# Performance work log

Hardware: AMD Instinct MI355X
Metric: run time of the kernel (lower is better)

The kernel has to match this reference:

```python
import jax, jax.numpy as jnp
import numpy as np
import math

S, B, H, NH = 2048, 1, 4096, 32
D = H // NH  # 128 head dim


def rotate_half(x):
    x1, x2 = x[..., : x.shape[-1] // 2], x[..., x.shape[-1] // 2 :]
    return jnp.concatenate((-x2, x1), axis=-1)


def setup_inputs() -> dict:
    key = jax.random.key(0)
    k1, k2, k3, k4, k5 = jax.random.split(key, 5)
    hidden_states = jax.random.normal(k1, (S, B, H), dtype=jnp.float32)
    position_ids = jnp.broadcast_to(jnp.arange(S, dtype=jnp.int32)[None, :], (B, S))
    # causal mask: True = masked (upper triangle above diagonal)
    attention_mask = jnp.triu(jnp.ones((S, S), dtype=bool), k=1)[None, None]
    W_qkv = jax.random.normal(k2, (H, 3 * H), dtype=jnp.float32) * 0.02
    b_qkv = jax.random.normal(k3, (3 * H,), dtype=jnp.float32) * 0.02
    W_dense = jax.random.normal(k4, (H, H), dtype=jnp.float32) * 0.02
    b_dense = jax.random.normal(k5, (H,), dtype=jnp.float32) * 0.02
    return {
        "hidden_states": hidden_states,
        "position_ids": position_ids,
        "attention_mask": attention_mask,
        "W_qkv": W_qkv,
        "b_qkv": b_qkv,
        "W_dense": W_dense,
        "b_dense": b_dense,
        "layer_id": 27,
    }


def reference(hidden_states, position_ids, attention_mask, W_qkv, b_qkv, W_dense, b_dense, layer_id):
    s, b, h = hidden_states.shape
    nh, d = NH, D
    # QKV projection: [s, b, 3h] -> [s, b, nh, 3d] -> split
    mixed = hidden_states @ W_qkv + b_qkv
    mixed = mixed.reshape(s, b, nh, 3 * d)
    q, k, v = jnp.split(mixed, 3, axis=-1)  # each [s, b, nh, d]
    # rotary embedding indexed by position_ids (transposed to [s, b])
    pos = position_ids.T  # [s, b]
    inv_freq = 1.0 / (10000.0 ** (jnp.arange(0, d, 2, dtype=jnp.float32) / d))
    freqs = pos[..., None].astype(jnp.float32) * inv_freq  # [s, b, d/2]
    emb = jnp.concatenate((freqs, freqs), axis=-1)  # [s, b, d]
    cos = jnp.cos(emb)[:, :, None, :]  # [s, b, 1, d]
    sin = jnp.sin(emb)[:, :, None, :]
    q = q * cos + rotate_half(q) * sin
    k = k * cos + rotate_half(k) * sin
    # attention with per-layer scaling coeff (cancels in softmax except mask fill)
    coeff = jnp.float32(layer_id + 1)
    q_scaled = q / (math.sqrt(d) * coeff)
    scores = jnp.einsum("sbnd,tbnd->bnst", q_scaled, k)  # [b, nh, s, s]
    scores = jnp.where(attention_mask, jnp.float32(-10000.0), scores) * coeff
    probs = jax.nn.softmax(scores, axis=-1)
    ctx = jnp.einsum("bnst,tbnd->sbnd", probs, v).reshape(s, b, h)
    out = ctx @ W_dense + b_dense
    return out
```

## Files before the change

kernel.cpp:

```cpp
#include <hip/hip_runtime.h>

#define S_LEN 2048
#define HID   4096
#define NHEAD 32
#define DHEAD 128
#define H3    12288

typedef __attribute__((ext_vector_type(8))) __bf16 bf16x8;
typedef __attribute__((ext_vector_type(4))) __bf16 bf16x4;
typedef __attribute__((ext_vector_type(4))) float  f32x4;

__device__ __forceinline__ void gl_lds16(const void* g, void* l) {
  __builtin_amdgcn_global_load_lds(
      (const __attribute__((address_space(1))) void*)g,
      (__attribute__((address_space(3))) void*)l, 16, 0, 0);
}

__global__ void cvt_f32_bf16(const float* __restrict__ in, __bf16* __restrict__ out, int n4) {
  int i = blockIdx.x * blockDim.x + threadIdx.x;
  if (i >= n4) return;
  float4 v = ((const float4*)in)[i];
  bf16x4 o;
  o.x = (__bf16)v.x; o.y = (__bf16)v.y; o.z = (__bf16)v.z; o.w = (__bf16)v.w;
  ((bf16x4*)out)[i] = o;
}

__global__ void transpose_cvt(const float* __restrict__ in, __bf16* __restrict__ out, int R, int C) {
  __shared__ float t[64][65];
  const int tid = threadIdx.x;
  const int r0 = blockIdx.y * 64, c0 = blockIdx.x * 64;
#pragma unroll
  for (int p = 0; p < 4; ++p) {
    int r = p * 16 + (tid >> 4);
    int c4 = (tid & 15) * 4;
    float4 v = *(const float4*)(in + (size_t)(r0 + r) * C + c0 + c4);
    t[r][c4] = v.x; t[r][c4 + 1] = v.y; t[r][c4 + 2] = v.z; t[r][c4 + 3] = v.w;
  }
  __syncthreads();
#pragma unroll
  for (int p = 0; p < 4; ++p) {
    int c = p * 16 + (tid >> 4);
    int rg = (tid & 15) * 4;
    bf16x4 o;
    o.x = (__bf16)t[rg][c]; o.y = (__bf16)t[rg + 1][c];
    o.z = (__bf16)t[rg + 2][c]; o.w = (__bf16)t[rg + 3][c];
    *(bf16x4*)(out + (size_t)(c0 + c) * R + r0 + rg) = o;
  }
}

__global__ void rope_kernel(__bf16* __restrict__ q, __bf16* __restrict__ k,
                            const int* __restrict__ pos) {
  int idx = blockIdx.x * 256 + threadIdx.x;
  int j = idx & 63;
  int hs = idx >> 6;
  int s = hs & (S_LEN - 1);
  float p = (float)pos[s];
  float invf = __expf(-(float)j * (9.210340371976184f / 64.f));
  float a = p * invf;
  float c, sn;
  __sincosf(a, &sn, &c);
  size_t base = (size_t)hs * 128;
  float x1 = (float)q[base + j], x2 = (float)q[base + j + 64];
  q[base + j]      = (__bf16)(x1 * c - x2 * sn);
  q[base + j + 64] = (__bf16)(x2 * c + x1 * sn);
  x1 = (float)k[base + j]; x2 = (float)k[base + j + 64];
  k[base + j]      = (__bf16)(x1 * c - x2 * sn);
  k[base + j + 64] = (__bf16)(x2 * c + x1 * sn);
}

template <int EPI>
__global__ __launch_bounds__(256, 2)
void gemm_bf16(const __bf16* __restrict__ A, const __bf16* __restrict__ BT,
               const float* __restrict__ bias, int K,
               __bf16* __restrict__ outq, __bf16* __restrict__ outk,
               __bf16* __restrict__ outvt, float* __restrict__ outf) {
  const int tid = threadIdx.x;
  const int lane = tid & 63;
  const int wave = tid >> 6;
  const int bm = blockIdx.x * 128;
  const int bn = blockIdx.y * 128;

  __shared__ __bf16 As[128 * 64];
  __shared__ __bf16 Bs[128 * 64];
  char* Ab = (char*)As;
  char* Bb = (char*)Bs;

  f32x4 acc[4][4] = {};

  const int wm = (wave >> 1) * 64;
  const int wn = (wave & 1) * 64;

  const int sr = tid >> 3;
  const int sc = (tid & 7) * 16;
  const int scs = sc ^ ((sr & 7) << 4);

  const char* Arow = (const char*)(A + (size_t)(bm + sr) * K) + scs;
  const char* Brow = (const char*)(BT + (size_t)(bn + sr) * K) + scs;

  for (int k0 = 0; k0 < K; k0 += 64) {
    const char* a_src = Arow + (size_t)k0 * 2;
    const char* b_src = Brow + (size_t)k0 * 2;
    char* a_dst = Ab + wave * 1024;
    char* b_dst = Bb + wave * 1024;
#pragma unroll
    for (int i = 0; i < 4; ++i) {
      gl_lds16(a_src + (size_t)i * 32 * K * 2, a_dst + i * 4096);
      gl_lds16(b_src + (size_t)i * 32 * K * 2, b_dst + i * 4096);
    }
    __syncthreads();
#pragma unroll
    for (int kk = 0; kk < 2; ++kk) {
      bf16x8 af[4], bfr[4];
#pragma unroll
      for (int m = 0; m < 4; ++m) {
        int row = wm + m * 16 + (lane & 15);
        int cb = (kk * 64 + ((lane >> 4) << 4)) ^ ((row & 7) << 4);
        af[m] = *(const bf16x8*)(Ab + row * 128 + cb);
      }
#pragma unroll
      for (int n = 0; n < 4; ++n) {
        int row = wn + n * 16 + (lane & 15);
        int cb = (kk * 64 + ((lane >> 4) << 4)) ^ ((row & 7) << 4);
        bfr[n] = *(const bf16x8*)(Bb + row * 128 + cb);
      }
#pragma unroll
      for (int m = 0; m < 4; ++m)
#pragma unroll
        for (int n = 0; n < 4; ++n)
          acc[m][n] = __builtin_amdgcn_mfma_f32_16x16x32_bf16(af[m], bfr[n], acc[m][n], 0, 0, 0);
    }
    __syncthreads();
  }

  const int rbase = (lane >> 4) << 2;
  const int cl = lane & 15;
  if (EPI == 0) {
    const int route = (bn >> 7) % 3;
    const int head = bn / 384;
#pragma unroll
    for (int n = 0; n < 4; ++n) {
      const int d = wn + n * 16 + cl;
      const float bv = bias[bn + d];
#pragma unroll
      for (int m = 0; m < 4; ++m) {
        const int srow = bm + wm + m * 16 + rbase;
        if (route == 2) {
          bf16x4 o;
          o.x = (__bf16)(acc[m][n][0] + bv);
          o.y = (__bf16)(acc[m][n][1] + bv);
          o.z = (__bf16)(acc[m][n][2] + bv);
          o.w = (__bf16)(acc[m][n][3] + bv);
          *(bf16x4*)(outvt + ((size_t)head * 128 + d) * S_LEN + srow) = o;
        } else {
          __bf16* dst = (route == 0 ? outq : outk) + (size_t)head * S_LEN * 128;
#pragma unroll
          for (int r = 0; r < 4; ++r)
            dst[(size_t)(srow + r) * 128 + d] = (__bf16)(acc[m][n][r] + bv);
        }
      }
    }
  } else {
#pragma unroll
    for (int n = 0; n < 4; ++n) {
      const int col = bn + wn + n * 16 + cl;
      const float bv = bias[col];
#pragma unroll
      for (int m = 0; m < 4; ++m) {
        const int srow = bm + wm + m * 16 + rbase;
#pragma unroll
        for (int r = 0; r < 4; ++r)
          outf[(size_t)(srow + r) * HID + col] = acc[m][n][r] + bv;
      }
    }
  }
}

__global__ __launch_bounds__(256, 2)
void attn_kernel(const __bf16* __restrict__ q, const __bf16* __restrict__ k,
                 const __bf16* __restrict__ vt, __bf16* __restrict__ ctx) {
  const int qb = blockIdx.x, h = blockIdx.y;
  const int tid = threadIdx.x, lane = tid & 63, wave = tid >> 6;
  __shared__ __bf16 Ks[64 * 128];
  __shared__ __bf16 Vs[128 * 64];
  __shared__ __bf16 Ps[4][32 * 64];
  char* Kb = (char*)Ks;
  char* Vb = (char*)Vs;
  char* Pb = (char*)(Ps[wave]);

  const __bf16* qh = q + (size_t)h * S_LEN * 128;
  const __bf16* kh = k + (size_t)h * S_LEN * 128;
  const __bf16* vh = vt + (size_t)h * 128 * S_LEN;

  const int qrow0 = qb * 128 + wave * 32;
  const int cl = lane & 15, rbase = (lane >> 4) << 2;

  bf16x8 qf[2][4];
#pragma unroll
  for (int m = 0; m < 2; ++m)
#pragma unroll
    for (int kk = 0; kk < 4; ++kk)
      qf[m][kk] = *(const bf16x8*)(qh + (size_t)(qrow0 + m * 16 + cl) * 128 + kk * 32 + ((lane >> 4) << 3));

  f32x4 oacc[2][8] = {};
  float mrow[2][4], lrow[2][4];
#pragma unroll
  for (int m = 0; m < 2; ++m)
#pragma unroll
    for (int r = 0; r < 4; ++r) { mrow[m][r] = -1e30f; lrow[m][r] = 0.f; }

  const int krow = tid >> 4, kcol = (tid & 15) * 16;
  const int kcs = kcol ^ ((krow & 7) << 4);
  const int vrow = tid >> 3, vcol = (tid & 7) * 16;
  const int vcs = vcol ^ ((vrow & 7) << 4);

  const int nT = 2 * qb + 2;
  for (int t = 0; t < nT; ++t) {
    {
      const char* src = (const char*)(kh + (size_t)(t * 64 + krow) * 128) + kcs;
      char* dst = Kb + wave * 1024;
#pragma unroll
      for (int i = 0; i < 4; ++i)
        gl_lds16(src + (size_t)i * 16 * 256, dst + i * 4096);
    }
    {
      const char* src = (const char*)(vh + (size_t)vrow * S_LEN + t * 64) + vcs;
      char* dst = Vb + wave * 1024;
#pragma unroll
      for (int i = 0; i < 4; ++i)
        gl_lds16(src + (size_t)i * 32 * (S_LEN * 2), dst + i * 4096);
    }
    __syncthreads();
    if (t * 64 <= qrow0 + 31) {
      f32x4 sacc[2][4] = {};
#pragma unroll
      for (int kk = 0; kk < 4; ++kk) {
        bf16x8 bk[4];
#pragma unroll
        for (int n = 0; n < 4; ++n) {
          int row = n * 16 + cl;
          int cb = (kk * 64 + ((lane >> 4) << 4)) ^ ((row & 7) << 4);
          bk[n] = *(const bf16x8*)(Kb + row * 256 + cb);
        }
#pragma unroll
        for (int m = 0; m < 2; ++m)
#pragma unroll
          for (int n = 0; n < 4; ++n)
            sacc[m][n] = __builtin_amdgcn_mfma_f32_16x16x32_bf16(qf[m][kk], bk[n], sacc[m][n], 0, 0, 0);
      }
#pragma unroll
      for (int m = 0; m < 2; ++m) {
        float pmax[4];
#pragma unroll
        for (int r = 0; r < 4; ++r) pmax[r] = -1e30f;
#pragma unroll
        for (int n = 0; n < 4; ++n) {
          const int col = t * 64 + n * 16 + cl;
#pragma unroll
          for (int r = 0; r < 4; ++r) {
            const int row = qrow0 + m * 16 + rbase + r;
            float sv = sacc[m][n][r] * 0.08838834764831845f;
            sv = (col > row) ? -1e30f : sv;
            sacc[m][n][r] = sv;
            pmax[r] = fmaxf(pmax[r], sv);
          }
        }
#pragma unroll
        for (int xm = 1; xm < 16; xm <<= 1)
#pragma unroll
          for (int r = 0; r < 4; ++r)
            pmax[r] = fmaxf(pmax[r], __shfl_xor(pmax[r], xm, 64));
#pragma unroll
        for (int r = 0; r < 4; ++r) {
          const float mnew = fmaxf(mrow[m][r], pmax[r]);
          const float alpha = __expf(mrow[m][r] - mnew);
          mrow[m][r] = mnew;
          float psum = 0.f;
#pragma unroll
          for (int n = 0; n < 4; ++n) {
            float p = __expf(sacc[m][n][r] - mnew);
            sacc[m][n][r] = p;
            psum += p;
          }
#pragma unroll
          for (int xm = 1; xm < 16; xm <<= 1)
            psum += __shfl_xor(psum, xm, 64);
          lrow[m][r] = lrow[m][r] * alpha + psum;
#pragma unroll
          for (int nd = 0; nd < 8; ++nd)
            oacc[m][nd][r] *= alpha;
        }
#pragma unroll
        for (int n = 0; n < 4; ++n) {
          const int colb = (n * 16 + cl) * 2;
#pragma unroll
          for (int r = 0; r < 4; ++r) {
            const int row = m * 16 + rbase + r;
            *(__bf16*)(Pb + row * 128 + (colb ^ ((row & 7) << 4))) = (__bf16)sacc[m][n][r];
          }
        }
      }
#pragma unroll
      for (int kk = 0; kk < 2; ++kk) {
        bf16x8 pa[2], bv[8];
#pragma unroll
        for (int m = 0; m < 2; ++m) {
          int row = m * 16 + cl;
          int cb = (kk * 64 + ((lane >> 4) << 4)) ^ ((row & 7) << 4);
          pa[m] = *(const bf16x8*)(Pb + row * 128 + cb);
        }
#pragma unroll
        for (int nd = 0; nd < 8; ++nd) {
          int row = nd * 16 + cl;
          int cb = (kk * 64 + ((lane >> 4) << 4)) ^ ((row & 7) << 4);
          bv[nd] = *(const bf16x8*)(Vb + row * 128 + cb);
        }
#pragma unroll
        for (int m = 0; m < 2; ++m)
#pragma unroll
          for (int nd = 0; nd < 8; ++nd)
            oacc[m][nd] = __builtin_amdgcn_mfma_f32_16x16x32_bf16(pa[m], bv[nd], oacc[m][nd], 0, 0, 0);
      }
    }
    __syncthreads();
  }
#pragma unroll
  for (int m = 0; m < 2; ++m)
#pragma unroll
    for (int nd = 0; nd < 8; ++nd) {
      const int d = nd * 16 + cl;
#pragma unroll
      for (int r = 0; r < 4; ++r) {
        const int srow = qrow0 + m * 16 + rbase + r;
        ctx[(size_t)srow * HID + h * 128 + d] = (__bf16)(oacc[m][nd][r] / lrow[m][r]);
      }
    }
}

extern "C" void kernel_launch(void* const* d_in, const int* in_sizes, int n_in,
                              void* d_out, int out_size, void* d_ws, size_t ws_size,
                              hipStream_t stream) {
  const float* hs = (const float*)d_in[0];
  const int* pos = (const int*)d_in[1];
  const float* wqkv = (const float*)d_in[3];
  const float* bqkv = (const float*)d_in[4];
  const float* wd = (const float*)d_in[5];
  const float* bd = (const float*)d_in[6];
  float* out = (float*)d_out;

  char* ws = (char*)d_ws;
  const size_t MB = 1024ull * 1024ull;
  if (ws_size < 160 * MB) return;
  __bf16* wT  = (__bf16*)(ws);
  __bf16* xb  = (__bf16*)(ws + 96 * MB);
  __bf16* qb_ = (__bf16*)(ws + 112 * MB);
  __bf16* kb_ = (__bf16*)(ws + 128 * MB);
  __bf16* vtb = (__bf16*)(ws + 144 * MB);

  cvt_f32_bf16<<<8192, 256, 0, stream>>>(hs, xb, 2097152);
  transpose_cvt<<<dim3(192, 64), 256, 0, stream>>>(wqkv, wT, 4096, 12288);
  gemm_bf16<0><<<dim3(16, 96), 256, 0, stream>>>(xb, wT, bqkv, 4096, qb_, kb_, vtb, nullptr);
  rope_kernel<<<16384, 256, 0, stream>>>(qb_, kb_, pos);
  transpose_cvt<<<dim3(64, 64), 256, 0, stream>>>(wd, wT, 4096, 4096);
  attn_kernel<<<dim3(16, 32), 256, 0, stream>>>(qb_, kb_, vtb, xb);
  gemm_bf16<1><<<dim3(16, 32), 256, 0, stream>>>(xb, wT, bd, 4096, nullptr, nullptr, nullptr, out);
}
```

Baseline: 509.5 us.

## Pair causal query tiles per attention block to balance work across blocks

Each attention block now handles two 64-row query tiles, p and 31-p, one after the other, instead of one 128-row tile. Every block therefore does about the same number of key tiles, removing the causal triangle's imbalance where late blocks set the critical path. Each wave now owns 16 query rows rather than 32, and the causal mask is applied only on the diagonal tile. In exchange, each loaded K/V tile is reused by fewer query rows, so MFMA work per sync and per LDS load is lower.

```diff
diff --git a/kernel.cpp b/kernel.cpp
--- a/kernel.cpp
+++ b/kernel.cpp
@@ -178,11 +178,11 @@
 __global__ __launch_bounds__(256, 2)
 void attn_kernel(const __bf16* __restrict__ q, const __bf16* __restrict__ k,
                  const __bf16* __restrict__ vt, __bf16* __restrict__ ctx) {
-  const int qb = blockIdx.x, h = blockIdx.y;
+  const int p = blockIdx.x, h = blockIdx.y;
   const int tid = threadIdx.x, lane = tid & 63, wave = tid >> 6;
   __shared__ __bf16 Ks[64 * 128];
   __shared__ __bf16 Vs[128 * 64];
-  __shared__ __bf16 Ps[4][32 * 64];
+  __shared__ __bf16 Ps[4][16 * 64];
   char* Kb = (char*)Ks;
   char* Vb = (char*)Vs;
   char* Pb = (char*)(Ps[wave]);
@@ -191,47 +191,45 @@
   const __bf16* kh = k + (size_t)h * S_LEN * 128;
   const __bf16* vh = vt + (size_t)h * 128 * S_LEN;
 
-  const int qrow0 = qb * 128 + wave * 32;
   const int cl = lane & 15, rbase = (lane >> 4) << 2;
-
-  bf16x8 qf[2][4];
-#pragma unroll
-  for (int m = 0; m < 2; ++m)
-#pragma unroll
-    for (int kk = 0; kk < 4; ++kk)
-      qf[m][kk] = *(const bf16x8*)(qh + (size_t)(qrow0 + m * 16 + cl) * 128 + kk * 32 + ((lane >> 4) << 3));
-
-  f32x4 oacc[2][8] = {};
-  float mrow[2][4], lrow[2][4];
-#pragma unroll
-  for (int m = 0; m < 2; ++m)
-#pragma unroll
-    for (int r = 0; r < 4; ++r) { mrow[m][r] = -1e30f; lrow[m][r] = 0.f; }
 
   const int krow = tid >> 4, kcol = (tid & 15) * 16;
   const int kcs = kcol ^ ((krow & 7) << 4);
   const int vrow = tid >> 3, vcol = (tid & 7) * 16;
   const int vcs = vcol ^ ((vrow & 7) << 4);
 
-  const int nT = 2 * qb + 2;
-  for (int t = 0; t < nT; ++t) {
-    {
-      const char* src = (const char*)(kh + (size_t)(t * 64 + krow) * 128) + kcs;
-      char* dst = Kb + wave * 1024;
-#pragma unroll
-      for (int i = 0; i < 4; ++i)
-        gl_lds16(src + (size_t)i * 16 * 256, dst + i * 4096);
-    }
-    {
-      const char* src = (const char*)(vh + (size_t)vrow * S_LEN + t * 64) + vcs;
-      char* dst = Vb + wave * 1024;
-#pragma unroll
-      for (int i = 0; i < 4; ++i)
-        gl_lds16(src + (size_t)i * 32 * (S_LEN * 2), dst + i * 4096);
-    }
-    __syncthreads();
-    if (t * 64 <= qrow0 + 31) {
-      f32x4 sacc[2][4] = {};
+  for (int half = 0; half < 2; ++half) {
+    const int qt = half ? (31 - p) : p;
+    const int qrow0 = qt * 64 + wave * 16;
+
+    bf16x8 qf[4];
+#pragma unroll
+    for (int kk = 0; kk < 4; ++kk)
+      qf[kk] = *(const bf16x8*)(qh + (size_t)(qrow0 + cl) * 128 + kk * 32 + ((lane >> 4) << 3));
+
+    f32x4 oacc[8] = {};
+    float mrow[4], lrow[4];
+#pragma unroll
+    for (int r = 0; r < 4; ++r) { mrow[r] = -1e30f; lrow[r] = 0.f; }
+
+    for (int j = 0; j <= qt; ++j) {
+      {
+        const char* src = (const char*)(kh + (size_t)(j * 64 + krow) * 128) + kcs;
+        char* dst = Kb + wave * 1024;
+#pragma unroll
+        for (int i = 0; i < 4; ++i)
+          gl_lds16(src + (size_t)i * 16 * 256, dst + i * 4096);
+      }
+      {
+        const char* src = (const char*)(vh + (size_t)vrow * S_LEN + j * 64) + vcs;
+        char* dst = Vb + wave * 1024;
+#pragma unroll
+        for (int i = 0; i < 4; ++i)
+          gl_lds16(src + (size_t)i * 32 * (S_LEN * 2), dst + i * 4096);
+      }
+      __syncthreads();
+
+      f32x4 sacc[4] = {};
 #pragma unroll
       for (int kk = 0; kk < 4; ++kk) {
         bf16x8 bk[4];
@@ -242,71 +240,79 @@
           bk[n] = *(const bf16x8*)(Kb + row * 256 + cb);
         }
 #pragma unroll
-        for (int m = 0; m < 2; ++m)
-#pragma unroll
-          for (int n = 0; n < 4; ++n)
-            sacc[m][n] = __builtin_amdgcn_mfma_f32_16x16x32_bf16(qf[m][kk], bk[n], sacc[m][n], 0, 0, 0);
-      }
-#pragma unroll
-      for (int m = 0; m < 2; ++m) {
-        float pmax[4];
-#pragma unroll
-        for (int r = 0; r < 4; ++r) pmax[r] = -1e30f;
+        for (int n = 0; n < 4; ++n)
+          sacc[n] = __builtin_amdgcn_mfma_f32_16x16x32_bf16(qf[kk], bk[n], sacc[n], 0, 0, 0);
+      }
+
+      float pmax[4];
+#pragma unroll
+      for (int r = 0; r < 4; ++r) pmax[r] = -1e30f;
+      if (j == qt) {
 #pragma unroll
         for (int n = 0; n < 4; ++n) {
-          const int col = t * 64 + n * 16 + cl;
+          const int col = n * 16 + cl;
 #pragma unroll
           for (int r = 0; r < 4; ++r) {
-            const int row = qrow0 + m * 16 + rbase + r;
-            float sv = sacc[m][n][r] * 0.08838834764831845f;
+            const int row = wave * 16 + rbase + r;
+            float sv = sacc[n][r] * 0.08838834764831845f;
             sv = (col > row) ? -1e30f : sv;
-            sacc[m][n][r] = sv;
+            sacc[n][r] = sv;
             pmax[r] = fmaxf(pmax[r], sv);
           }
         }
+      } else {
+#pragma unroll
+        for (int n = 0; n < 4; ++n)
+#pragma unroll
+          for (int r = 0; r < 4; ++r) {
+            float sv = sacc[n][r] * 0.08838834764831845f;
+            sacc[n][r] = sv;
+            pmax[r] = fmaxf(pmax[r], sv);
+          }
+      }
+#pragma unroll
+      for (int xm = 1; xm < 16; xm <<= 1)
+#pragma unroll
+        for (int r = 0; r < 4; ++r)
+          pmax[r] = fmaxf(pmax[r], __shfl_xor(pmax[r], xm, 64));
+#pragma unroll
+      for (int r = 0; r < 4; ++r) {
+        const float mnew = fmaxf(mrow[r], pmax[r]);
+        const float alpha = __expf(mrow[r] - mnew);
+        mrow[r] = mnew;
+        float psum = 0.f;
+#pragma unroll
+        for (int n = 0; n < 4; ++n) {
+          float pe = __expf(sacc[n][r] - mnew);
+          sacc[n][r] = pe;
+          psum += pe;
+        }
 #pragma unroll
         for (int xm = 1; xm < 16; xm <<= 1)
-#pragma unroll
-          for (int r = 0; r < 4; ++r)
-            pmax[r] = fmaxf(pmax[r], __shfl_xor(pmax[r], xm, 64));
+          psum += __shfl_xor(psum, xm, 64);
+        lrow[r] = lrow[r] * alpha + psum;
+#pragma unroll
+        for (int nd = 0; nd < 8; ++nd)
+          oacc[nd][r] *= alpha;
+      }
+
+#pragma unroll
+      for (int n = 0; n < 4; ++n) {
+        const int colb = (n * 16 + cl) * 2;
 #pragma unroll
         for (int r = 0; r < 4; ++r) {
-          const float mnew = fmaxf(mrow[m][r], pmax[r]);
-          const float alpha = __expf(mrow[m][r] - mnew);
-          mrow[m][r] = mnew;
-          float psum = 0.f;
-#pragma unroll
-          for (int n = 0; n < 4; ++n) {
-            float p = __expf(sacc[m][n][r] - mnew);
-            sacc[m][n][r] = p;
-            psum += p;
-          }
-#pragma unroll
-          for (int xm = 1; xm < 16; xm <<= 1)
-            psum += __shfl_xor(psum, xm, 64);
-          lrow[m][r] = lrow[m][r] * alpha + psum;
-#pragma unroll
-          for (int nd = 0; nd < 8; ++nd)
-            oacc[m][nd][r] *= alpha;
-        }
-#pragma unroll
-        for (int n = 0; n < 4; ++n) {
-          const int colb = (n * 16 + cl) * 2;
-#pragma unroll
-          for (int r = 0; r < 4; ++r) {
-            const int row = m * 16 + rbase + r;
-            *(__bf16*)(Pb + row * 128 + (colb ^ ((row & 7) << 4))) = (__bf16)sacc[m][n][r];
-          }
-        }
-      }
+          const int row = rbase + r;
+          *(__bf16*)(Pb + row * 128 + (colb ^ ((row & 7) << 4))) = (__bf16)sacc[n][r];
+        }
+      }
+
 #pragma unroll
       for (int kk = 0; kk < 2; ++kk) {
-        bf16x8 pa[2], bv[8];
-#pragma unroll
-        for (int m = 0; m < 2; ++m) {
-          int row = m * 16 + cl;
+        bf16x8 pa, bv[8];
+        {
+          int row = cl;
           int cb = (kk * 64 + ((lane >> 4) << 4)) ^ ((row & 7) << 4);
-          pa[m] = *(const bf16x8*)(Pb + row * 128 + cb);
+          pa = *(const bf16x8*)(Pb + row * 128 + cb);
         }
 #pragma unroll
         for (int nd = 0; nd < 8; ++nd) {
@@ -315,25 +321,22 @@
           bv[nd] = *(const bf16x8*)(Vb + row * 128 + cb);
         }
 #pragma unroll
-        for (int m = 0; m < 2; ++m)
-#pragma unroll
-          for (int nd = 0; nd < 8; ++nd)
-            oacc[m][nd] = __builtin_amdgcn_mfma_f32_16x16x32_bf16(pa[m], bv[nd], oacc[m][nd], 0, 0, 0);
-      }
-    }
-    __syncthreads();
-  }
-#pragma unroll
-  for (int m = 0; m < 2; ++m)
+        for (int nd = 0; nd < 8; ++nd)
+          oacc[nd] = __builtin_amdgcn_mfma_f32_16x16x32_bf16(pa, bv[nd], oacc[nd], 0, 0, 0);
+      }
+      __syncthreads();
+    }
+
 #pragma unroll
     for (int nd = 0; nd < 8; ++nd) {
       const int d = nd * 16 + cl;
 #pragma unroll
       for (int r = 0; r < 4; ++r) {
-        const int srow = qrow0 + m * 16 + rbase + r;
-        ctx[(size_t)srow * HID + h * 128 + d] = (__bf16)(oacc[m][nd][r] / lrow[m][r]);
-      }
-    }
+        const int srow = qrow0 + rbase + r;
+        ctx[(size_t)srow * HID + h * 128 + d] = (__bf16)(oacc[nd][r] / lrow[r]);
+      }
+    }
+  }
 }
 
 extern "C" void kernel_launch(void* const* d_in, const int* in_sizes, int n_in,
```

After: 462.4 us. 9.2% less time.
